# Kernel tuning notes

Hardware: AMD Instinct MI355X
Metric: run time of the kernel (lower is better)

The kernel has to match this reference:

```python
import jax, jax.numpy as jnp
import numpy as np

N = 12288
INPUT_DIM = 128
OUTPUT_DIM = 64
ALPHA = 0.2  # LeakyReLU negative slope


def setup_inputs() -> dict:
    key = jax.random.key(0)
    k_h, k_W, k_a = jax.random.split(key, 3)
    h = jax.random.normal(k_h, (N, INPUT_DIM), dtype=jnp.float32)
    # xavier_uniform with gain=1.414 for W [input_dim, output_dim]
    limW = 1.414 * np.sqrt(6.0 / (INPUT_DIM + OUTPUT_DIM))
    W = jax.random.uniform(k_W, (INPUT_DIM, OUTPUT_DIM), dtype=jnp.float32,
                           minval=-limW, maxval=limW)
    # xavier_uniform for a [2*output_dim, 1]
    lima = 1.414 * np.sqrt(6.0 / (2 * OUTPUT_DIM + 1))
    a = jax.random.uniform(k_a, (2 * OUTPUT_DIM, 1), dtype=jnp.float32,
                           minval=-lima, maxval=lima)
    return {"h": h, "W": W, "a": a}


def reference(h, W, a):
    Wh = h @ W                                  # [N, d_out]
    Wh1 = Wh @ a[:OUTPUT_DIM, :]                # [N, 1]
    Wh2 = Wh @ a[OUTPUT_DIM:, :]                # [N, 1]
    e = Wh1 + Wh2.T                             # [N, N] broadcast add
    e = jax.nn.leaky_relu(e, negative_slope=ALPHA)
    attention = jax.nn.softmax(e, axis=1)       # row-wise softmax
    # eval mode: dropout is identity
    h_prime = attention @ Wh                    # [N, d_out]
    return jax.nn.elu(h_prime)
```

## Files before the change

kernel.cpp:

```cpp
#include <hip/hip_runtime.h>

#define N 12288
#define M (2 * N)
#define DIN 128
#define DOUT 64
#define NBIN 8192
#define BSHIFT 19
#define NCHUNK 384
#define K1BLKS 768

__device__ __forceinline__ unsigned f_ord(float x) {
    unsigned b = __float_as_uint(x);
    return (b & 0x80000000u) ? ~b : (b | 0x80000000u);
}
__device__ __forceinline__ float ord_f(unsigned u) {
    unsigned b = (u & 0x80000000u) ? (u & 0x7FFFFFFFu) : ~u;
    return __uint_as_float(b);
}
__device__ __forceinline__ int t_bin(float x) { return (int)(f_ord(x) >> BSHIFT); }

struct Args {
    const float *h, *W, *a;
    float *Wh, *s, *t, *tblkmax, *Thdr;
    unsigned long long *vals64;
    float *tfin;
    int *idfin, *binstart;
    float2 *VU, *sc;
    float2 *baseVU, *basesc;
    float *utot, *utots;
    float *out;
};

__global__ __launch_bounds__(256) void k1_gemm(Args A) {
    __shared__ float4 sm4[2576];
    __shared__ float wmax[4];
    int tid = threadIdx.x, lane = tid & 63, wave = tid >> 6, blk = blockIdx.x;
    float4* Ws4 = sm4;
    float4* hs4 = sm4 + 2048;
    const float4* W4 = (const float4*)A.W;
    #pragma unroll
    for (int e = tid; e < 2048; e += 256) Ws4[e] = W4[e];
    int row0 = blk * 16;
    const float4* h4 = (const float4*)(A.h + (size_t)row0 * DIN);
    #pragma unroll
    for (int e = tid; e < 512; e += 256) hs4[(e >> 5) * 33 + (e & 31)] = h4[e];
    __syncthreads();
    int c0 = tid & 15, r = tid >> 4;
    float4 acc = make_float4(0.f, 0.f, 0.f, 0.f);
    #pragma unroll 4
    for (int kk = 0; kk < 32; ++kk) {
        float4 hv = hs4[r * 33 + kk];
        float4 w0 = Ws4[(4 * kk + 0) * 16 + c0];
        float4 w1 = Ws4[(4 * kk + 1) * 16 + c0];
        float4 w2 = Ws4[(4 * kk + 2) * 16 + c0];
        float4 w3 = Ws4[(4 * kk + 3) * 16 + c0];
        acc.x = fmaf(hv.x, w0.x, acc.x); acc.y = fmaf(hv.x, w0.y, acc.y);
        acc.z = fmaf(hv.x, w0.z, acc.z); acc.w = fmaf(hv.x, w0.w, acc.w);
        acc.x = fmaf(hv.y, w1.x, acc.x); acc.y = fmaf(hv.y, w1.y, acc.y);
        acc.z = fmaf(hv.y, w1.z, acc.z); acc.w = fmaf(hv.y, w1.w, acc.w);
        acc.x = fmaf(hv.z, w2.x, acc.x); acc.y = fmaf(hv.z, w2.y, acc.y);
        acc.z = fmaf(hv.z, w2.z, acc.z); acc.w = fmaf(hv.z, w2.w, acc.w);
        acc.x = fmaf(hv.w, w3.x, acc.x); acc.y = fmaf(hv.w, w3.y, acc.y);
        acc.z = fmaf(hv.w, w3.z, acc.z); acc.w = fmaf(hv.w, w3.w, acc.w);
    }
    int row = row0 + r;
    ((float4*)A.Wh)[(size_t)row * 16 + c0] = acc;
    float4 a1 = ((const float4*)A.a)[c0];
    float4 a2 = ((const float4*)A.a)[16 + c0];
    float sv = acc.x * a1.x + acc.y * a1.y + acc.z * a1.z + acc.w * a1.w;
    float tv = acc.x * a2.x + acc.y * a2.y + acc.z * a2.z + acc.w * a2.w;
    #pragma unroll
    for (int off = 8; off; off >>= 1) {
        sv += __shfl_xor(sv, off, 64);
        tv += __shfl_xor(tv, off, 64);
    }
    if (c0 == 0) { A.s[row] = sv; A.t[row] = tv; }
    float tmax = tv;
    tmax = fmaxf(tmax, __shfl_xor(tmax, 16, 64));
    tmax = fmaxf(tmax, __shfl_xor(tmax, 32, 64));
    if (lane == 0) wmax[wave] = tmax;
    __syncthreads();
    if (tid == 0)
        A.tblkmax[blk] = fmaxf(fmaxf(wmax[0], wmax[1]), fmaxf(wmax[2], wmax[3]));
}

__global__ __launch_bounds__(1024) void k2_sort(Args A) {
    __shared__ int hist0[NBIN];
    __shared__ int hist1[NBIN];
    __shared__ int pre[NBIN];
    __shared__ int wtot[16];
    __shared__ float fmax_[16];
    int tid = threadIdx.x, lane = tid & 63, wave = tid >> 6, blk = blockIdx.x;
    #pragma unroll
    for (int e = tid; e < NBIN; e += 1024) { hist0[e] = 0; hist1[e] = 0; pre[e] = 0; }
    __syncthreads();
    int my0 = blk * 1024;
    int* myhist = (wave & 1) ? hist1 : hist0;
    #pragma unroll
    for (int it = 0; it < 6; ++it) {
        int qi = it * 1024 + tid;
        int e4 = qi * 4;
        float4 v4;
        if (it < 3) {
            v4 = ((const float4*)A.t)[qi];
        } else {
            float4 s4 = ((const float4*)A.s)[qi - 3072];
            v4 = make_float4(-s4.x, -s4.y, -s4.z, -s4.w);
        }
        int ba = t_bin(v4.x), bb = t_bin(v4.y), bc = t_bin(v4.z), bd = t_bin(v4.w);
        atomicAdd(&myhist[ba], 1); atomicAdd(&myhist[bb], 1);
        atomicAdd(&myhist[bc], 1); atomicAdd(&myhist[bd], 1);
        if (e4 < my0) {
            atomicAdd(&pre[ba], 1); atomicAdd(&pre[bb], 1);
            atomicAdd(&pre[bc], 1); atomicAdd(&pre[bd], 1);
        }
    }
    __syncthreads();
    int b0 = tid * 8;
    int c8[8]; int sum = 0;
    #pragma unroll
    for (int g = 0; g < 8; ++g) { c8[g] = sum; sum += hist0[b0 + g] + hist1[b0 + g]; }
    int inc = sum;
    #pragma unroll
    for (int off = 1; off < 64; off <<= 1) {
        int nb = __shfl_up(inc, off, 64);
        if (lane >= off) inc += nb;
    }
    if (lane == 63) wtot[wave] = inc;
    __syncthreads();
    int wbase = 0;
    #pragma unroll
    for (int w = 0; w < 16; ++w) wbase += (w < wave) ? wtot[w] : 0;
    int tstart = wbase + inc - sum;
    #pragma unroll
    for (int g = 0; g < 8; ++g) {
        int bs = tstart + c8[g];
        pre[b0 + g] += bs;
        A.binstart[b0 + g] = bs;
    }
    if (tid == 0 && blk == 0) A.binstart[NBIN] = M;
    float m = (tid < K1BLKS) ? A.tblkmax[tid] : -3.4e38f;
    #pragma unroll
    for (int off = 32; off; off >>= 1) m = fmaxf(m, __shfl_xor(m, off, 64));
    if (lane == 0) fmax_[wave] = m;
    __syncthreads();
    if (tid == 0) {
        float mm = fmax_[0];
        #pragma unroll
        for (int w = 1; w < 16; ++w) mm = fmaxf(mm, fmax_[w]);
        A.Thdr[0] = mm;
    }
    __syncthreads();
    {
        int e = my0 + tid;
        float v = (e < N) ? A.t[e] : -A.s[e - N];
        int pi = (e < N) ? (e + N) : (e - N);
        int pos = atomicAdd(&pre[t_bin(v)], 1);
        A.vals64[pos] = ((unsigned long long)f_ord(v) << 32) | (unsigned)pi;
    }
}

__global__ __launch_bounds__(256) void k3_rank(Args A) {
    __shared__ int parts[256];
    int tid = threadIdx.x;
    int li = tid & 15, sub = tid >> 4;
    int p = blockIdx.x * 16 + li;
    unsigned long long kp = A.vals64[p];
    int b = (int)(kp >> (32 + BSHIFT));
    int lo = A.binstart[b], hi = A.binstart[b + 1];
    int len = hi - lo;
    int qlen = (len + 15) >> 4;
    int qlo = lo + sub * qlen;
    if (qlo > hi) qlo = hi;
    int qhi = qlo + qlen;
    if (qhi > hi) qhi = hi;
    int cnt = 0;
    int q = qlo;
    while (q < qhi && (q & 3)) cnt += (int)(A.vals64[q++] < kp);
    int bend = q + ((qhi - q) & ~3);
    #pragma unroll 2
    for (; q < bend; q += 4) {
        ulonglong2 u0 = *(const ulonglong2*)&A.vals64[q];
        ulonglong2 u1 = *(const ulonglong2*)&A.vals64[q + 2];
        cnt += (int)(u0.x < kp) + (int)(u0.y < kp)
             + (int)(u1.x < kp) + (int)(u1.y < kp);
    }
    while (q < qhi) cnt += (int)(A.vals64[q++] < kp);
    parts[sub * 16 + li] = cnt;
    __syncthreads();
    if (sub == 0) {
        int tot = 0;
        #pragma unroll
        for (int s2 = 0; s2 < 16; ++s2) tot += parts[s2 * 16 + li];
        int pi = (int)(unsigned)(kp & 0xffffffffu);
        A.tfin[lo + tot] = ord_f((unsigned)(kp >> 32));
        A.idfin[lo + tot] = (pi >= N) ? (pi - N) : (pi + N);
    }
}

__global__ __launch_bounds__(64) void k4_sums(Args A) {
    int lane = threadIdx.x;
    int c = blockIdx.x;
    float T = A.Thdr[0];
    float myval = A.tfin[c * 64 + lane];
    int myid = A.idfin[c * 64 + lane];
    float wvm = 0.f, wum = 0.f;
    if (myid < N) {
        wvm = __expf(0.2f * (myval - T));
        float w2 = wvm * wvm, w4 = w2 * w2;
        wum = w4 * wvm;
    }
    float av = 0.f, au = 0.f, svs = 0.f, sus = 0.f;
    #pragma unroll
    for (int k = 0; k < 64; ++k) {
        int uid = __shfl(myid, k, 64);
        float xv = (uid < N) ? A.Wh[(size_t)uid * DOUT + lane] : 0.f;
        float wv = __shfl(wvm, k, 64);
        float wu = __shfl(wum, k, 64);
        av = fmaf(wv, xv, av); au = fmaf(wu, xv, au);
        svs += wv; sus += wu;
    }
    A.VU[(size_t)lane * NCHUNK + c] = make_float2(av, au);
    if (lane == 0) A.sc[c] = make_float2(svs, sus);
}

__global__ __launch_bounds__(256) void k4b_scan(Args A) {
    int tid = threadIdx.x, wave = tid >> 6, lane = tid & 63;
    int task = blockIdx.x * 4 + wave;
    if (task >= 65) return;
    const float2* srcp; float2* dstp;
    if (task < 64) { srcp = A.VU + (size_t)task * NCHUNK; dstp = A.baseVU + (size_t)task * NCHUNK; }
    else           { srcp = A.sc;                          dstp = A.basesc; }
    float2 xs[6];
    #pragma unroll
    for (int b = 0; b < 6; ++b) xs[b] = srcp[b * 64 + lane];
    float bv = 0.f, bu = 0.f;
    #pragma unroll
    for (int b = 0; b < 6; ++b) {
        float iv = xs[b].x, iu = xs[b].y;
        #pragma unroll
        for (int off = 1; off < 64; off <<= 1) {
            float nv = __shfl_up(iv, off, 64);
            float nu = __shfl_up(iu, off, 64);
            if (lane >= off) { iv += nv; iu += nu; }
        }
        dstp[b * 64 + lane] = make_float2(bv + iv - xs[b].x, bu + iu - xs[b].y);
        bv += __shfl(iv, 63, 64);
        bu += __shfl(iu, 63, 64);
    }
    if (lane == 0) {
        if (task < 64) A.utot[task] = bu;
        else           A.utots[0] = bu;
    }
}

__global__ __launch_bounds__(64) void k5_apply(Args A) {
    int lane = threadIdx.x;
    int c = blockIdx.x;
    float T = A.Thdr[0];
    float myval = A.tfin[c * 64 + lane];
    int myid = A.idfin[c * 64 + lane];
    float2 bvu = A.baseVU[(size_t)lane * NCHUNK + c];
    float x[64];
    #pragma unroll
    for (int k = 0; k < 64; ++k) {
        int uid = __shfl(myid, k, 64);
        x[k] = (uid < N) ? A.Wh[(size_t)uid * DOUT + lane] : 0.f;
    }
    float wvm = 0.f, wum = 0.f;
    if (myid < N) {
        wvm = __expf(0.2f * (myval - T));
        float w2 = wvm * wvm, w4 = w2 * w2;
        wum = w4 * wvm;
    }
    unsigned long long keymask = __ballot(myid < N);
    float2 bsc = A.basesc[c];
    float rv = bvu.x, ru = bvu.y, rvs = bsc.x, rus = bsc.y;
    float tu  = A.utot[lane];
    float tus = A.utots[0];
    #pragma unroll
    for (int k = 0; k < 64; ++k) {
        if ((keymask >> k) & 1) {
            float wv = __shfl(wvm, k, 64);
            float wu = __shfl(wum, k, 64);
            rv = fmaf(wv, x[k], rv); ru = fmaf(wu, x[k], ru);
            rvs += wv; rus += wu;
        } else {
            float uval = __shfl(myval, k, 64);
            int uid = __shfl(myid, k, 64);
            int i = uid - N;
            float xx = -uval + T;
            float mm = fmaxf(xx, 0.2f * xx);
            float cp_ = __expf(xx - mm);
            float cn_ = __expf(0.2f * xx - mm);
            float num = cn_ * rv + cp_ * (tu - ru);
            float den = cn_ * rvs + cp_ * (tus - rus);
            float r = __fdividef(num, den);
            A.out[(size_t)i * DOUT + lane] = r > 0.f ? r : (__expf(r) - 1.f);
        }
    }
}

extern "C" void kernel_launch(void* const* d_in, const int* in_sizes, int n_in,
                              void* d_out, int out_size, void* d_ws, size_t ws_size,
                              hipStream_t stream) {
    float* ws = (float*)d_ws;
    size_t o = 0;
    Args A;
    A.h = (const float*)d_in[0];
    A.W = (const float*)d_in[1];
    A.a = (const float*)d_in[2];
    A.out = (float*)d_out;
    A.Wh      = ws + o; o += (size_t)N * DOUT;
    A.s       = ws + o; o += N;
    A.t       = ws + o; o += N;
    A.tblkmax = ws + o; o += K1BLKS;
    A.Thdr    = ws + o; o += 16;
    A.vals64  = (unsigned long long*)(ws + o); o += 2 * (size_t)M;
    A.tfin    = ws + o; o += M;
    A.VU      = (float2*)(ws + o); o += 2 * (size_t)DOUT * NCHUNK;
    A.sc      = (float2*)(ws + o); o += 2 * NCHUNK;
    A.baseVU  = (float2*)(ws + o); o += 2 * (size_t)DOUT * NCHUNK;
    A.basesc  = (float2*)(ws + o); o += 2 * NCHUNK;
    A.utot    = ws + o; o += DOUT;
    A.utots   = ws + o; o += 16;
    A.idfin    = (int*)(ws + o); o += M;
    A.binstart = (int*)(ws + o); o += NBIN + 16;

    k1_gemm <<<K1BLKS, 256, 0, stream>>>(A);
    k2_sort <<<24, 1024, 0, stream>>>(A);
    k3_rank <<<M / 16, 256, 0, stream>>>(A);
    k4_sums <<<NCHUNK, 64, 0, stream>>>(A);
    k4b_scan<<<17, 256, 0, stream>>>(A);
    k5_apply<<<NCHUNK, 64, 0, stream>>>(A);
}
```

Before: 101.6 us.

## Split k4_sums and k5_apply chunk work across four waves per block

k4_sums and k5_apply now launch 256-thread blocks instead of 64. Each of the four waves handles 16 of a chunk's 64 sorted keys, and partial sums go through shared memory. In k5 each wave first builds a local prefix from its own keys, then adds the partials of earlier waves before doing its sequential apply. The aim is more parallelism and shorter serial dependency chains on only 384 blocks, plus a smaller x register array. The cost is a block barrier and some redundant shuffles and exps.

```diff
diff --git a/kernel.cpp b/kernel.cpp
--- a/kernel.cpp
+++ b/kernel.cpp
@@ -198,8 +198,10 @@
     }
 }
 
-__global__ __launch_bounds__(64) void k4_sums(Args A) {
-    int lane = threadIdx.x;
+__global__ __launch_bounds__(256) void k4_sums(Args A) {
+    __shared__ float2 part[4][64];
+    __shared__ float2 scp[4];
+    int tid = threadIdx.x, wave = tid >> 6, lane = tid & 63;
     int c = blockIdx.x;
     float T = A.Thdr[0];
     float myval = A.tfin[c * 64 + lane];
@@ -211,8 +213,10 @@
         wum = w4 * wvm;
     }
     float av = 0.f, au = 0.f, svs = 0.f, sus = 0.f;
-    #pragma unroll
-    for (int k = 0; k < 64; ++k) {
+    int k0 = wave * 16;
+    #pragma unroll
+    for (int kk = 0; kk < 16; ++kk) {
+        int k = k0 + kk;
         int uid = __shfl(myid, k, 64);
         float xv = (uid < N) ? A.Wh[(size_t)uid * DOUT + lane] : 0.f;
         float wv = __shfl(wvm, k, 64);
@@ -220,8 +224,19 @@
         av = fmaf(wv, xv, av); au = fmaf(wu, xv, au);
         svs += wv; sus += wu;
     }
-    A.VU[(size_t)lane * NCHUNK + c] = make_float2(av, au);
-    if (lane == 0) A.sc[c] = make_float2(svs, sus);
+    part[wave][lane] = make_float2(av, au);
+    if (lane == 0) scp[wave] = make_float2(svs, sus);
+    __syncthreads();
+    if (wave == 0) {
+        float2 p1 = part[1][lane], p2 = part[2][lane], p3 = part[3][lane];
+        A.VU[(size_t)lane * NCHUNK + c] =
+            make_float2(av + p1.x + p2.x + p3.x, au + p1.y + p2.y + p3.y);
+        if (lane == 0) {
+            float2 s1 = scp[1], s2 = scp[2], s3 = scp[3];
+            A.sc[c] = make_float2(svs + s1.x + s2.x + s3.x,
+                                  sus + s1.y + s2.y + s3.y);
+        }
+    }
 }
 
 __global__ __launch_bounds__(256) void k4b_scan(Args A) {
@@ -254,19 +269,15 @@
     }
 }
 
-__global__ __launch_bounds__(64) void k5_apply(Args A) {
-    int lane = threadIdx.x;
+__global__ __launch_bounds__(256) void k5_apply(Args A) {
+    __shared__ float2 part[4][64];
+    __shared__ float2 scp[4];
+    int tid = threadIdx.x, wave = tid >> 6, lane = tid & 63;
     int c = blockIdx.x;
     float T = A.Thdr[0];
     float myval = A.tfin[c * 64 + lane];
     int myid = A.idfin[c * 64 + lane];
     float2 bvu = A.baseVU[(size_t)lane * NCHUNK + c];
-    float x[64];
-    #pragma unroll
-    for (int k = 0; k < 64; ++k) {
-        int uid = __shfl(myid, k, 64);
-        x[k] = (uid < N) ? A.Wh[(size_t)uid * DOUT + lane] : 0.f;
-    }
     float wvm = 0.f, wum = 0.f;
     if (myid < N) {
         wvm = __expf(0.2f * (myval - T));
@@ -274,16 +285,41 @@
         wum = w4 * wvm;
     }
     unsigned long long keymask = __ballot(myid < N);
+    int k0 = wave * 16;
+    float x[16];
+    float pav = 0.f, pau = 0.f, psv = 0.f, psu = 0.f;
+    #pragma unroll
+    for (int kk = 0; kk < 16; ++kk) {
+        int k = k0 + kk;
+        int uid = __shfl(myid, k, 64);
+        x[kk] = (uid < N) ? A.Wh[(size_t)uid * DOUT + lane] : 0.f;
+        float wv = __shfl(wvm, k, 64);
+        float wu = __shfl(wum, k, 64);
+        pav = fmaf(wv, x[kk], pav); pau = fmaf(wu, x[kk], pau);
+        psv += wv; psu += wu;
+    }
+    part[wave][lane] = make_float2(pav, pau);
+    if (lane == 0) scp[wave] = make_float2(psv, psu);
+    __syncthreads();
     float2 bsc = A.basesc[c];
     float rv = bvu.x, ru = bvu.y, rvs = bsc.x, rus = bsc.y;
+    #pragma unroll
+    for (int w2 = 0; w2 < 3; ++w2) {
+        if (w2 < wave) {
+            float2 p = part[w2][lane];
+            float2 s = scp[w2];
+            rv += p.x; ru += p.y; rvs += s.x; rus += s.y;
+        }
+    }
     float tu  = A.utot[lane];
     float tus = A.utots[0];
     #pragma unroll
-    for (int k = 0; k < 64; ++k) {
+    for (int kk = 0; kk < 16; ++kk) {
+        int k = k0 + kk;
         if ((keymask >> k) & 1) {
             float wv = __shfl(wvm, k, 64);
             float wu = __shfl(wum, k, 64);
-            rv = fmaf(wv, x[k], rv); ru = fmaf(wu, x[k], ru);
+            rv = fmaf(wv, x[kk], rv); ru = fmaf(wu, x[kk], ru);
             rvs += wv; rus += wu;
         } else {
             float uval = __shfl(myval, k, 64);
@@ -330,7 +366,7 @@
     k1_gemm <<<K1BLKS, 256, 0, stream>>>(A);
     k2_sort <<<24, 1024, 0, stream>>>(A);
     k3_rank <<<M / 16, 256, 0, stream>>>(A);
-    k4_sums <<<NCHUNK, 64, 0, stream>>>(A);
+    k4_sums <<<NCHUNK, 256, 0, stream>>>(A);
     k4b_scan<<<17, 256, 0, stream>>>(A);
-    k5_apply<<<NCHUNK, 64, 0, stream>>>(A);
-}
+    k5_apply<<<NCHUNK, 256, 0, stream>>>(A);
+}
```

New measurement: 91.67 us, median of 3. 9.8% less time.
